# Performance work log

Measured on AMD Instinct MI355X. Metric: run time of the kernel, lower is better.

Reference implementation:

```python
import jax, jax.numpy as jnp
import numpy as np

N_NODES = 100000
N_EDGES = 1600000
IN_C, HID_C, OUT_C = 128, 128, 64


def setup_inputs() -> dict:
    key = jax.random.key(0)
    k1, k2, k3, k4 = jax.random.split(key, 4)
    x = jax.random.normal(k1, (N_NODES, IN_C), dtype=jnp.float32)
    edge_index = jax.random.randint(k2, (2, N_EDGES), 0, N_NODES, dtype=jnp.int32)
    # Glorot-ish init for linear weights, zero bias (PyG GCNConv default bias=0)
    W1 = jax.random.normal(k3, (IN_C, HID_C), dtype=jnp.float32) / np.sqrt(IN_C)
    b1 = jnp.zeros((HID_C,), dtype=jnp.float32)
    W2 = jax.random.normal(k4, (HID_C, OUT_C), dtype=jnp.float32) / np.sqrt(HID_C)
    b2 = jnp.zeros((OUT_C,), dtype=jnp.float32)
    return {"x": x, "edge_index": edge_index, "W1": W1, "b1": b1, "W2": W2, "b2": b2}


def gcn_conv(x, edge_index, W, b, n_nodes):
    """PyG GCNConv: out = D^{-1/2} (A + I) D^{-1/2} (x W) + b."""
    h = x @ W  # [N, C_out]
    loop = jnp.arange(n_nodes, dtype=edge_index.dtype)
    src = jnp.concatenate([edge_index[0], loop])  # messages flow src -> dst
    dst = jnp.concatenate([edge_index[1], loop])
    # degree at destination nodes (includes self-loops)
    deg = jax.ops.segment_sum(jnp.ones_like(src, dtype=h.dtype), dst,
                              num_segments=n_nodes)
    dis = jnp.where(deg > 0, jax.lax.rsqrt(jnp.maximum(deg, 1e-12)), 0.0)
    norm = dis[src] * dis[dst]  # [E+N]
    msg = h[src] * norm[:, None]  # gather + scale
    out = jax.ops.segment_sum(msg, dst, num_segments=n_nodes)  # scatter-add
    return out + b


def reference(x, edge_index, W1, b1, W2, b2):
    h = jax.nn.relu(gcn_conv(x, edge_index, W1, b1, N_NODES))
    return gcn_conv(h, edge_index, W2, b2, N_NODES)
```

## Files before the change

kernel.cpp:

```cpp
#include <hip/hip_runtime.h>

#define N_NODES 100000
#define N_EDGES 1600000
#define IN_C 128
#define HID_C 128
#define OUT_C 64

#define SH 8
#define NBKT 391
#define CAP 4608
#define EPB 4096
#define EPT 16

typedef __attribute__((ext_vector_type(8))) short bf16x8;
typedef __attribute__((ext_vector_type(4))) float f32x4;

static __device__ __forceinline__ unsigned f2bf(float f) {
  union { float f; unsigned u; } v; v.f = f;
  unsigned r = v.u + 0x7fffu + ((v.u >> 16) & 1u);
  return r >> 16;
}
static __device__ __forceinline__ float bf2f(unsigned hu) {
  union { unsigned u; float f; } v; v.u = hu << 16; return v.f;
}
static __device__ __forceinline__ float bflo(unsigned u) {
  union { unsigned u; float f; } v; v.u = u << 16; return v.f;
}
static __device__ __forceinline__ float bfhi(unsigned u) {
  union { unsigned u; float f; } v; v.u = u & 0xffff0000u; return v.f;
}


__global__ __launch_bounds__(256) void k_partA(const int* __restrict__ src,
                                               const int* __restrict__ dst,
                                               int* __restrict__ bcnt,
                                               unsigned* __restrict__ tmp, int e) {
  __shared__ unsigned stage[EPB];
  __shared__ unsigned short bid[EPB];
  __shared__ int hist[NBKT];
  __shared__ int lstart[NBKT];
  __shared__ int base[NBKT];
  __shared__ int ps[256];
  const int t = threadIdx.x;
  const int e0 = blockIdx.x * EPB;
  const int m = (e0 + EPB < e ? EPB : e - e0);

  for (int i = t; i < NBKT; i += 256) hist[i] = 0;
  __syncthreads();

  int rsrc[EPT], rdst[EPT];
#pragma unroll
  for (int i = 0; i < EPT; ++i) {
    int idx = e0 + i * 256 + t;
    if (idx < e) {
      rsrc[i] = src[idx];
      rdst[i] = dst[idx];
      atomicAdd(&hist[rdst[i] >> SH], 1);
    }
  }
  __syncthreads();

  int a0 = (2 * t < NBKT) ? hist[2 * t] : 0;
  int a1 = (2 * t + 1 < NBKT) ? hist[2 * t + 1] : 0;
  ps[t] = a0 + a1;
  __syncthreads();
  for (int off = 1; off < 256; off <<= 1) {
    int add = (t >= off) ? ps[t - off] : 0;
    __syncthreads();
    ps[t] += add;
    __syncthreads();
  }
  int ex = ps[t] - (a0 + a1);
  if (2 * t < NBKT) lstart[2 * t] = ex;
  if (2 * t + 1 < NBKT) lstart[2 * t + 1] = ex + a0;

  for (int i = t; i < NBKT; i += 256) {
    int h = hist[i];
    base[i] = h ? atomicAdd(&bcnt[i], h) : 0;
    hist[i] = 0;
  }
  __syncthreads();

#pragma unroll
  for (int i = 0; i < EPT; ++i) {
    int idx = e0 + i * 256 + t;
    if (idx < e) {
      int d = rdst[i];
      int b = d >> SH;
      int pos = lstart[b] + atomicAdd(&hist[b], 1);
      stage[pos] = (unsigned)rsrc[i] | ((unsigned)(d & 255) << 17);
      bid[pos] = (unsigned short)b;
    }
  }
  __syncthreads();

  for (int pos = t; pos < m; pos += 256) {
    int b = bid[pos];
    int slot = base[b] + (pos - lstart[b]);
    if (slot < CAP)
      tmp[(size_t)b * CAP + slot] = stage[pos];
  }
}

__global__ __launch_bounds__(256) void k_cnt_scan(const unsigned* __restrict__ tmp,
                                                  const int* __restrict__ bcnt,
                                                  int* __restrict__ rowptr,
                                                  int* __restrict__ bsums,
                                                  float* __restrict__ dis, int n) {
  __shared__ int h[256];
  __shared__ int s[256];
  const int b = blockIdx.x, t = threadIdx.x;
  h[t] = 0;
  __syncthreads();
  int m = bcnt[b];
  if (m > CAP) m = CAP;
  for (int j = t; j < m; j += 256)
    atomicAdd(&h[tmp[(size_t)b * CAP + j] >> 17], 1);
  __syncthreads();
  const int node = (b << SH) + t;
  int v = (node < n) ? h[t] : 0;
  if (node < n) dis[node] = rsqrtf((float)(v + 1));
  s[t] = v;
  __syncthreads();
  for (int off = 1; off < 256; off <<= 1) {
    int add = (t >= off) ? s[t - off] : 0;
    __syncthreads();
    s[t] += add;
    __syncthreads();
  }
  if (node < n) rowptr[node] = s[t] - v;
  if (t == 255) bsums[b] = s[255];
}

__global__ void k_scan_sums(int* __restrict__ bsums, int nb) {
  __shared__ int s[512];
  int t = threadIdx.x;
  int v = (t < nb) ? bsums[t] : 0;
  s[t] = v;
  __syncthreads();
  for (int off = 1; off < 512; off <<= 1) {
    int add = (t >= off) ? s[t - off] : 0;
    __syncthreads();
    s[t] += add;
    __syncthreads();
  }
  if (t < nb) bsums[t] = s[t] - v;
}

__global__ void k_add_off(int* __restrict__ rowptr, const int* __restrict__ bsums,
                          int n, int e) {
  int i = blockIdx.x * blockDim.x + threadIdx.x;
  if (i < n) rowptr[i] += bsums[i >> 8];
  else if (i == n) rowptr[n] = e;
}

__global__ __launch_bounds__(256) void k_partB(const unsigned* __restrict__ tmp,
                                               const int* __restrict__ bcnt,
                                               const int* __restrict__ rowptr,
                                               int* __restrict__ col, int n) {
  __shared__ int cur[256];
  const int b = blockIdx.x;
  const int t = threadIdx.x;
  const int node = (b << SH) + t;
  cur[t] = (node < n) ? rowptr[node] : 0;
  __syncthreads();
  int m = bcnt[b];
  if (m > CAP) m = CAP;
  for (int j = t; j < m; j += 256) {
    unsigned v = tmp[(size_t)b * CAP + j];
    int pos = atomicAdd(&cur[v >> 17], 1);
    col[pos] = (int)(v & 0x1FFFFu);
  }
}


__global__ void k_prepW(const float* __restrict__ W1, const float* __restrict__ W2,
                        unsigned short* __restrict__ W1h, unsigned short* __restrict__ W1l,
                        unsigned short* __restrict__ W2h, unsigned short* __restrict__ W2l) {
  int i = blockIdx.x * blockDim.x + threadIdx.x;
  if (i < IN_C * HID_C) {
    int k = i >> 7, c = i & 127;
    float w = W1[i];
    unsigned hi = f2bf(w);
    W1h[c * 128 + k] = (unsigned short)hi;
    W1l[c * 128 + k] = (unsigned short)f2bf(w - bf2f(hi));
  }
  int j = i - IN_C * HID_C;
  if (j >= 0 && j < HID_C * OUT_C) {
    int k = j >> 6, c = j & 63;
    float w = W2[j];
    unsigned hi = f2bf(w);
    W2h[c * 128 + k] = (unsigned short)hi;
    W2l[c * 128 + k] = (unsigned short)f2bf(w - bf2f(hi));
  }
}


__global__ __launch_bounds__(256) void k_mfma1(const float* __restrict__ X,
                                               const unsigned short* __restrict__ Wh,
                                               const unsigned short* __restrict__ Wl,
                                               const float* __restrict__ dis,
                                               unsigned short* __restrict__ Hs, int n) {
  __shared__ unsigned short xs[64 * 136];
  const int t = threadIdx.x;
  const int w = t >> 6, l = t & 63;
  const int lr = l & 15, lk = (l >> 4) * 8;
  const int row0 = blockIdx.x * 64;

  bf16x8 Bh[2][4], Bl[2][4];
#pragma unroll
  for (int c2 = 0; c2 < 2; ++c2)
#pragma unroll
    for (int kb = 0; kb < 4; ++kb) {
      int colw = w * 32 + c2 * 16 + lr;
      Bh[c2][kb] = *(const bf16x8*)&Wh[(size_t)colw * 128 + kb * 32 + lk];
      Bl[c2][kb] = *(const bf16x8*)&Wl[(size_t)colw * 128 + kb * 32 + lk];
    }

  for (int i = t; i < 64 * 32; i += 256) {
    int r = i >> 5, q = i & 31;
    float4 v = make_float4(0.f, 0.f, 0.f, 0.f);
    if (row0 + r < n) v = ((const float4*)(X + (size_t)(row0 + r) * IN_C))[q];
    unsigned p0 = f2bf(v.x) | (f2bf(v.y) << 16);
    unsigned p1 = f2bf(v.z) | (f2bf(v.w) << 16);
    *(uint2*)&xs[r * 136 + q * 4] = make_uint2(p0, p1);
  }
  __syncthreads();

#pragma unroll
  for (int rst = 0; rst < 4; ++rst) {
    bf16x8 a[4];
#pragma unroll
    for (int kb = 0; kb < 4; ++kb)
      a[kb] = *(const bf16x8*)&xs[(rst * 16 + lr) * 136 + kb * 32 + lk];
    f32x4 acc0 = (f32x4){0.f, 0.f, 0.f, 0.f};
    f32x4 acc1 = (f32x4){0.f, 0.f, 0.f, 0.f};
#pragma unroll
    for (int kb = 0; kb < 4; ++kb) {
      acc0 = __builtin_amdgcn_mfma_f32_16x16x32_bf16(a[kb], Bh[0][kb], acc0, 0, 0, 0);
      acc1 = __builtin_amdgcn_mfma_f32_16x16x32_bf16(a[kb], Bh[1][kb], acc1, 0, 0, 0);
      acc0 = __builtin_amdgcn_mfma_f32_16x16x32_bf16(a[kb], Bl[0][kb], acc0, 0, 0, 0);
      acc1 = __builtin_amdgcn_mfma_f32_16x16x32_bf16(a[kb], Bl[1][kb], acc1, 0, 0, 0);
    }
    const int rbase = row0 + rst * 16 + (l >> 4) * 4;
    float dv[4];
#pragma unroll
    for (int j = 0; j < 4; ++j) dv[j] = (rbase + j < n) ? dis[rbase + j] : 0.f;
#pragma unroll
    for (int c2 = 0; c2 < 2; ++c2) {
      int colw = w * 32 + c2 * 16 + lr;
      const f32x4& acc = c2 ? acc1 : acc0;
#pragma unroll
      for (int j = 0; j < 4; ++j) {
        int row = rbase + j;
        if (row < n) Hs[(size_t)row * HID_C + colw] = (unsigned short)f2bf(acc[j] * dv[j]);
      }
    }
  }
}


__global__ __launch_bounds__(256) void k_mfma2(const unsigned* __restrict__ G,
                                               const unsigned short* __restrict__ Wh,
                                               const unsigned short* __restrict__ Wl,
                                               const float* __restrict__ dis,
                                               unsigned short* __restrict__ Hs, int n) {
  __shared__ unsigned short xs[64 * 136];
  const int t = threadIdx.x;
  const int w = t >> 6, l = t & 63;
  const int lr = l & 15, lk = (l >> 4) * 8;
  const int row0 = blockIdx.x * 64;

  bf16x8 Bh[4], Bl[4];
#pragma unroll
  for (int kb = 0; kb < 4; ++kb) {
    int colw = w * 16 + lr;
    Bh[kb] = *(const bf16x8*)&Wh[(size_t)colw * 128 + kb * 32 + lk];
    Bl[kb] = *(const bf16x8*)&Wl[(size_t)colw * 128 + kb * 32 + lk];
  }

  for (int i = t; i < 64 * 32; i += 256) {
    int r = i >> 5, q = i & 31;
    uint2 v = make_uint2(0u, 0u);
    if (row0 + r < n) v = *(const uint2*)&G[(size_t)(row0 + r) * 64 + q * 2];
    *(uint2*)&xs[r * 136 + q * 4] = v;
  }
  __syncthreads();

#pragma unroll
  for (int rst = 0; rst < 4; ++rst) {
    bf16x8 a[4];
#pragma unroll
    for (int kb = 0; kb < 4; ++kb)
      a[kb] = *(const bf16x8*)&xs[(rst * 16 + lr) * 136 + kb * 32 + lk];
    f32x4 acc = (f32x4){0.f, 0.f, 0.f, 0.f};
#pragma unroll
    for (int kb = 0; kb < 4; ++kb) {
      acc = __builtin_amdgcn_mfma_f32_16x16x32_bf16(a[kb], Bh[kb], acc, 0, 0, 0);
      acc = __builtin_amdgcn_mfma_f32_16x16x32_bf16(a[kb], Bl[kb], acc, 0, 0, 0);
    }
    const int rbase = row0 + rst * 16 + (l >> 4) * 4;
    const int colw = w * 16 + lr;
#pragma unroll
    for (int j = 0; j < 4; ++j) {
      int row = rbase + j;
      if (row < n) Hs[(size_t)row * OUT_C + colw] =
          (unsigned short)f2bf(acc[j] * dis[row]);
    }
  }
}


__global__ __launch_bounds__(256) void k_agg128(const unsigned* __restrict__ Hs,
                                                const int* __restrict__ rowptr,
                                                const int* __restrict__ col,
                                                const float* __restrict__ dis,
                                                const float* __restrict__ bias,
                                                unsigned* __restrict__ G, int n) {
  const int node = (blockIdx.x * blockDim.x + threadIdx.x) >> 6;
  const int lane = threadIdx.x & 63;
  if (node >= n) return;
  const int g = lane >> 4, q = lane & 15;
  float a0 = 0.f, a1 = 0.f, a2 = 0.f, a3 = 0.f, a4 = 0.f, a5 = 0.f, a6 = 0.f, a7 = 0.f;
  const int beg = rowptr[node], end = rowptr[node + 1];
  int j = beg + g;
  for (; j + 8 <= end; j += 8) {
    int s0 = col[j], s1 = col[j + 4];
    uint4 v0 = *(const uint4*)&Hs[(size_t)s0 * 64 + q * 4];
    uint4 v1 = *(const uint4*)&Hs[(size_t)s1 * 64 + q * 4];
    a0 += bflo(v0.x) + bflo(v1.x); a1 += bfhi(v0.x) + bfhi(v1.x);
    a2 += bflo(v0.y) + bflo(v1.y); a3 += bfhi(v0.y) + bfhi(v1.y);
    a4 += bflo(v0.z) + bflo(v1.z); a5 += bfhi(v0.z) + bfhi(v1.z);
    a6 += bflo(v0.w) + bflo(v1.w); a7 += bfhi(v0.w) + bfhi(v1.w);
  }
  for (; j < end; j += 4) {
    int s = col[j];
    uint4 v = *(const uint4*)&Hs[(size_t)s * 64 + q * 4];
    a0 += bflo(v.x); a1 += bfhi(v.x);
    a2 += bflo(v.y); a3 += bfhi(v.y);
    a4 += bflo(v.z); a5 += bfhi(v.z);
    a6 += bflo(v.w); a7 += bfhi(v.w);
  }
  a0 += __shfl_xor(a0, 16, 64); a0 += __shfl_xor(a0, 32, 64);
  a1 += __shfl_xor(a1, 16, 64); a1 += __shfl_xor(a1, 32, 64);
  a2 += __shfl_xor(a2, 16, 64); a2 += __shfl_xor(a2, 32, 64);
  a3 += __shfl_xor(a3, 16, 64); a3 += __shfl_xor(a3, 32, 64);
  a4 += __shfl_xor(a4, 16, 64); a4 += __shfl_xor(a4, 32, 64);
  a5 += __shfl_xor(a5, 16, 64); a5 += __shfl_xor(a5, 32, 64);
  a6 += __shfl_xor(a6, 16, 64); a6 += __shfl_xor(a6, 32, 64);
  a7 += __shfl_xor(a7, 16, 64); a7 += __shfl_xor(a7, 32, 64);
  uint4 sv = *(const uint4*)&Hs[(size_t)node * 64 + q * 4];
  const float di = dis[node];
  const int c0 = q * 8;
  float2 b0 = *(const float2*)&bias[c0];
  float2 b1 = *(const float2*)&bias[c0 + 2];
  float2 b2 = *(const float2*)&bias[c0 + 4];
  float2 b3 = *(const float2*)&bias[c0 + 6];
  float r0 = fmaxf(fmaf(a0 + bflo(sv.x), di, b0.x), 0.f);
  float r1 = fmaxf(fmaf(a1 + bfhi(sv.x), di, b0.y), 0.f);
  float r2 = fmaxf(fmaf(a2 + bflo(sv.y), di, b1.x), 0.f);
  float r3 = fmaxf(fmaf(a3 + bfhi(sv.y), di, b1.y), 0.f);
  float r4 = fmaxf(fmaf(a4 + bflo(sv.z), di, b2.x), 0.f);
  float r5 = fmaxf(fmaf(a5 + bfhi(sv.z), di, b2.y), 0.f);
  float r6 = fmaxf(fmaf(a6 + bflo(sv.w), di, b3.x), 0.f);
  float r7 = fmaxf(fmaf(a7 + bfhi(sv.w), di, b3.y), 0.f);
  if (g == 0) {
    uint4 pk;
    pk.x = f2bf(r0) | (f2bf(r1) << 16);
    pk.y = f2bf(r2) | (f2bf(r3) << 16);
    pk.z = f2bf(r4) | (f2bf(r5) << 16);
    pk.w = f2bf(r6) | (f2bf(r7) << 16);
    *(uint4*)&G[(size_t)node * 64 + q * 4] = pk;
  }
}

__global__ __launch_bounds__(256) void k_agg64(const unsigned* __restrict__ Hs,
                                               const int* __restrict__ rowptr,
                                               const int* __restrict__ col,
                                               const float* __restrict__ dis,
                                               const float* __restrict__ bias,
                                               float* __restrict__ out, int n) {
  const int node = (blockIdx.x * blockDim.x + threadIdx.x) >> 6;
  const int lane = threadIdx.x & 63;
  if (node >= n) return;
  const int g = lane >> 4, q = lane & 15;
  float a0 = 0.f, a1 = 0.f, a2 = 0.f, a3 = 0.f;
  const int beg = rowptr[node], end = rowptr[node + 1];
  int j = beg + g;
  for (; j + 8 <= end; j += 8) {
    int s0 = col[j], s1 = col[j + 4];
    uint2 v0 = *(const uint2*)&Hs[(size_t)s0 * 32 + q * 2];
    uint2 v1 = *(const uint2*)&Hs[(size_t)s1 * 32 + q * 2];
    a0 += bflo(v0.x) + bflo(v1.x); a1 += bfhi(v0.x) + bfhi(v1.x);
    a2 += bflo(v0.y) + bflo(v1.y); a3 += bfhi(v0.y) + bfhi(v1.y);
  }
  for (; j < end; j += 4) {
    int s = col[j];
    uint2 v = *(const uint2*)&Hs[(size_t)s * 32 + q * 2];
    a0 += bflo(v.x); a1 += bfhi(v.x);
    a2 += bflo(v.y); a3 += bfhi(v.y);
  }
  a0 += __shfl_xor(a0, 16, 64); a0 += __shfl_xor(a0, 32, 64);
  a1 += __shfl_xor(a1, 16, 64); a1 += __shfl_xor(a1, 32, 64);
  a2 += __shfl_xor(a2, 16, 64); a2 += __shfl_xor(a2, 32, 64);
  a3 += __shfl_xor(a3, 16, 64); a3 += __shfl_xor(a3, 32, 64);
  uint2 sv = *(const uint2*)&Hs[(size_t)node * 32 + q * 2];
  const float di = dis[node];
  const int c0 = q * 4;
  float2 b0 = *(const float2*)&bias[c0];
  float2 b1 = *(const float2*)&bias[c0 + 2];
  if (g == 0) {
    float4 r;
    r.x = fmaf(a0 + bflo(sv.x), di, b0.x);
    r.y = fmaf(a1 + bfhi(sv.x), di, b0.y);
    r.z = fmaf(a2 + bflo(sv.y), di, b1.x);
    r.w = fmaf(a3 + bfhi(sv.y), di, b1.y);
    *(float4*)&out[(size_t)node * 64 + c0] = r;
  }
}


extern "C" void kernel_launch(void* const* d_in, const int* in_sizes, int n_in,
                              void* d_out, int out_size, void* d_ws, size_t ws_size,
                              hipStream_t stream) {
  const float* x  = (const float*)d_in[0];
  const int*   ei = (const int*)d_in[1];
  const float* W1 = (const float*)d_in[2];
  const float* b1 = (const float*)d_in[3];
  const float* W2 = (const float*)d_in[4];
  const float* b2 = (const float*)d_in[5];
  float* out = (float*)d_out;

  const int N = N_NODES, E = N_EDGES;
  const int* esrc = ei;
  const int* edst = ei + E;

  char* w = (char*)d_ws;
  auto alloc = [&](size_t bytes) -> char* {
    char* p = w;
    w += (bytes + 255) & ~(size_t)255;
    return p;
  };
  float* dis          = (float*)alloc((size_t)N * 4);
  int* rowptr         = (int*)alloc((size_t)(N + 1) * 4);
  int* bcnt           = (int*)alloc((size_t)NBKT * 4);
  int* bsums          = (int*)alloc(512 * 4);
  int* col            = (int*)alloc((size_t)E * 4);
  unsigned* tmp       = (unsigned*)alloc((size_t)NBKT * CAP * 4);
  unsigned short* h1s = (unsigned short*)alloc((size_t)N * HID_C * 2);
  unsigned* g1        = (unsigned*)alloc((size_t)N * (HID_C / 2) * 4);
  unsigned short* h2s = (unsigned short*)alloc((size_t)N * OUT_C * 2);
  unsigned short* W1h = (unsigned short*)alloc((size_t)IN_C * HID_C * 2);
  unsigned short* W1l = (unsigned short*)alloc((size_t)IN_C * HID_C * 2);
  unsigned short* W2h = (unsigned short*)alloc((size_t)HID_C * OUT_C * 2);
  unsigned short* W2l = (unsigned short*)alloc((size_t)HID_C * OUT_C * 2);

  hipMemsetAsync(bcnt, 0, (size_t)NBKT * 4, stream);
  k_partA<<<(E + EPB - 1) / EPB, 256, 0, stream>>>(esrc, edst, bcnt, tmp, E);
  k_cnt_scan<<<NBKT, 256, 0, stream>>>(tmp, bcnt, rowptr, bsums, dis, N);
  k_scan_sums<<<1, 512, 0, stream>>>(bsums, NBKT);
  k_add_off<<<(N + 1 + 255) / 256, 256, 0, stream>>>(rowptr, bsums, N, E);
  k_partB<<<NBKT, 256, 0, stream>>>(tmp, bcnt, rowptr, col, N);
  k_prepW<<<(IN_C * HID_C + HID_C * OUT_C + 255) / 256, 256, 0, stream>>>(
      W1, W2, W1h, W1l, W2h, W2l);

  k_mfma1<<<(N + 63) / 64, 256, 0, stream>>>(x, W1h, W1l, dis, h1s, N);
  k_agg128<<<(N * 64 + 255) / 256, 256, 0, stream>>>((const unsigned*)h1s, rowptr, col,
                                                     dis, b1, g1, N);
  k_mfma2<<<(N + 63) / 64, 256, 0, stream>>>(g1, W2h, W2l, dis, h2s, N);
  k_agg64<<<(N * 64 + 255) / 256, 256, 0, stream>>>((const unsigned*)h2s, rowptr, col,
                                                    dis, b2, out, N);
}
```

Measured before the change: 220.5 us.

## Unroll aggregation gathers, halve threads per node in agg64, widen partB

The 128-channel aggregation now unrolls to four independent row gathers per iteration, which puts more loads in flight. The 64-channel aggregation maps each node to 32 lanes instead of 64, so two edge groups per node replace four, with a 4-way unroll and a single shuffle reduction. The CSR fill kernel runs with 512 threads per block. More in-flight loads per lane could raise register pressure, and the agg64 remap halves the number of lanes working on each node's edge list.

Result: faster. 211.7 us (-4.0%).

```diff
diff --git a/kernel.cpp b/kernel.cpp
--- a/kernel.cpp
+++ b/kernel.cpp
@@ -154,19 +154,21 @@
   else if (i == n) rowptr[n] = e;
 }
 
-__global__ __launch_bounds__(256) void k_partB(const unsigned* __restrict__ tmp,
+__global__ __launch_bounds__(512) void k_partB(const unsigned* __restrict__ tmp,
                                                const int* __restrict__ bcnt,
                                                const int* __restrict__ rowptr,
                                                int* __restrict__ col, int n) {
   __shared__ int cur[256];
   const int b = blockIdx.x;
   const int t = threadIdx.x;
-  const int node = (b << SH) + t;
-  cur[t] = (node < n) ? rowptr[node] : 0;
+  if (t < 256) {
+    const int node = (b << SH) + t;
+    cur[t] = (node < n) ? rowptr[node] : 0;
+  }
   __syncthreads();
   int m = bcnt[b];
   if (m > CAP) m = CAP;
-  for (int j = t; j < m; j += 256) {
+  for (int j = t; j < m; j += 512) {
     unsigned v = tmp[(size_t)b * CAP + j];
     int pos = atomicAdd(&cur[v >> 17], 1);
     col[pos] = (int)(v & 0x1FFFFu);
@@ -324,14 +326,20 @@
   float a0 = 0.f, a1 = 0.f, a2 = 0.f, a3 = 0.f, a4 = 0.f, a5 = 0.f, a6 = 0.f, a7 = 0.f;
   const int beg = rowptr[node], end = rowptr[node + 1];
   int j = beg + g;
-  for (; j + 8 <= end; j += 8) {
-    int s0 = col[j], s1 = col[j + 4];
+  for (; j + 16 <= end; j += 16) {
+    int s0 = col[j], s1 = col[j + 4], s2 = col[j + 8], s3 = col[j + 12];
     uint4 v0 = *(const uint4*)&Hs[(size_t)s0 * 64 + q * 4];
     uint4 v1 = *(const uint4*)&Hs[(size_t)s1 * 64 + q * 4];
-    a0 += bflo(v0.x) + bflo(v1.x); a1 += bfhi(v0.x) + bfhi(v1.x);
-    a2 += bflo(v0.y) + bflo(v1.y); a3 += bfhi(v0.y) + bfhi(v1.y);
-    a4 += bflo(v0.z) + bflo(v1.z); a5 += bfhi(v0.z) + bfhi(v1.z);
-    a6 += bflo(v0.w) + bflo(v1.w); a7 += bfhi(v0.w) + bfhi(v1.w);
+    uint4 v2 = *(const uint4*)&Hs[(size_t)s2 * 64 + q * 4];
+    uint4 v3 = *(const uint4*)&Hs[(size_t)s3 * 64 + q * 4];
+    a0 += (bflo(v0.x) + bflo(v1.x)) + (bflo(v2.x) + bflo(v3.x));
+    a1 += (bfhi(v0.x) + bfhi(v1.x)) + (bfhi(v2.x) + bfhi(v3.x));
+    a2 += (bflo(v0.y) + bflo(v1.y)) + (bflo(v2.y) + bflo(v3.y));
+    a3 += (bfhi(v0.y) + bfhi(v1.y)) + (bfhi(v2.y) + bfhi(v3.y));
+    a4 += (bflo(v0.z) + bflo(v1.z)) + (bflo(v2.z) + bflo(v3.z));
+    a5 += (bfhi(v0.z) + bfhi(v1.z)) + (bfhi(v2.z) + bfhi(v3.z));
+    a6 += (bflo(v0.w) + bflo(v1.w)) + (bflo(v2.w) + bflo(v3.w));
+    a7 += (bfhi(v0.w) + bfhi(v1.w)) + (bfhi(v2.w) + bfhi(v3.w));
   }
   for (; j < end; j += 4) {
     int s = col[j];
@@ -356,15 +364,15 @@
   float2 b1 = *(const float2*)&bias[c0 + 2];
   float2 b2 = *(const float2*)&bias[c0 + 4];
   float2 b3 = *(const float2*)&bias[c0 + 6];
-  float r0 = fmaxf(fmaf(a0 + bflo(sv.x), di, b0.x), 0.f);
-  float r1 = fmaxf(fmaf(a1 + bfhi(sv.x), di, b0.y), 0.f);
-  float r2 = fmaxf(fmaf(a2 + bflo(sv.y), di, b1.x), 0.f);
-  float r3 = fmaxf(fmaf(a3 + bfhi(sv.y), di, b1.y), 0.f);
-  float r4 = fmaxf(fmaf(a4 + bflo(sv.z), di, b2.x), 0.f);
-  float r5 = fmaxf(fmaf(a5 + bfhi(sv.z), di, b2.y), 0.f);
-  float r6 = fmaxf(fmaf(a6 + bflo(sv.w), di, b3.x), 0.f);
-  float r7 = fmaxf(fmaf(a7 + bfhi(sv.w), di, b3.y), 0.f);
   if (g == 0) {
+    float r0 = fmaxf(fmaf(a0 + bflo(sv.x), di, b0.x), 0.f);
+    float r1 = fmaxf(fmaf(a1 + bfhi(sv.x), di, b0.y), 0.f);
+    float r2 = fmaxf(fmaf(a2 + bflo(sv.y), di, b1.x), 0.f);
+    float r3 = fmaxf(fmaf(a3 + bfhi(sv.y), di, b1.y), 0.f);
+    float r4 = fmaxf(fmaf(a4 + bflo(sv.z), di, b2.x), 0.f);
+    float r5 = fmaxf(fmaf(a5 + bfhi(sv.z), di, b2.y), 0.f);
+    float r6 = fmaxf(fmaf(a6 + bflo(sv.w), di, b3.x), 0.f);
+    float r7 = fmaxf(fmaf(a7 + bfhi(sv.w), di, b3.y), 0.f);
     uint4 pk;
     pk.x = f2bf(r0) | (f2bf(r1) << 16);
     pk.y = f2bf(r2) | (f2bf(r3) << 16);
@@ -380,30 +388,34 @@
                                                const float* __restrict__ dis,
                                                const float* __restrict__ bias,
                                                float* __restrict__ out, int n) {
-  const int node = (blockIdx.x * blockDim.x + threadIdx.x) >> 6;
-  const int lane = threadIdx.x & 63;
+  const int node = (blockIdx.x * blockDim.x + threadIdx.x) >> 5;
+  const int sub = threadIdx.x & 31;
   if (node >= n) return;
-  const int g = lane >> 4, q = lane & 15;
+  const int g = sub >> 4, q = sub & 15;
   float a0 = 0.f, a1 = 0.f, a2 = 0.f, a3 = 0.f;
   const int beg = rowptr[node], end = rowptr[node + 1];
   int j = beg + g;
   for (; j + 8 <= end; j += 8) {
-    int s0 = col[j], s1 = col[j + 4];
+    int s0 = col[j], s1 = col[j + 2], s2 = col[j + 4], s3 = col[j + 6];
     uint2 v0 = *(const uint2*)&Hs[(size_t)s0 * 32 + q * 2];
     uint2 v1 = *(const uint2*)&Hs[(size_t)s1 * 32 + q * 2];
-    a0 += bflo(v0.x) + bflo(v1.x); a1 += bfhi(v0.x) + bfhi(v1.x);
-    a2 += bflo(v0.y) + bflo(v1.y); a3 += bfhi(v0.y) + bfhi(v1.y);
-  }
-  for (; j < end; j += 4) {
+    uint2 v2 = *(const uint2*)&Hs[(size_t)s2 * 32 + q * 2];
+    uint2 v3 = *(const uint2*)&Hs[(size_t)s3 * 32 + q * 2];
+    a0 += (bflo(v0.x) + bflo(v1.x)) + (bflo(v2.x) + bflo(v3.x));
+    a1 += (bfhi(v0.x) + bfhi(v1.x)) + (bfhi(v2.x) + bfhi(v3.x));
+    a2 += (bflo(v0.y) + bflo(v1.y)) + (bflo(v2.y) + bflo(v3.y));
+    a3 += (bfhi(v0.y) + bfhi(v1.y)) + (bfhi(v2.y) + bfhi(v3.y));
+  }
+  for (; j < end; j += 2) {
     int s = col[j];
     uint2 v = *(const uint2*)&Hs[(size_t)s * 32 + q * 2];
     a0 += bflo(v.x); a1 += bfhi(v.x);
     a2 += bflo(v.y); a3 += bfhi(v.y);
   }
-  a0 += __shfl_xor(a0, 16, 64); a0 += __shfl_xor(a0, 32, 64);
-  a1 += __shfl_xor(a1, 16, 64); a1 += __shfl_xor(a1, 32, 64);
-  a2 += __shfl_xor(a2, 16, 64); a2 += __shfl_xor(a2, 32, 64);
-  a3 += __shfl_xor(a3, 16, 64); a3 += __shfl_xor(a3, 32, 64);
+  a0 += __shfl_xor(a0, 16, 64);
+  a1 += __shfl_xor(a1, 16, 64);
+  a2 += __shfl_xor(a2, 16, 64);
+  a3 += __shfl_xor(a3, 16, 64);
   uint2 sv = *(const uint2*)&Hs[(size_t)node * 32 + q * 2];
   const float di = dis[node];
   const int c0 = q * 4;
@@ -460,7 +472,7 @@
   k_cnt_scan<<<NBKT, 256, 0, stream>>>(tmp, bcnt, rowptr, bsums, dis, N);
   k_scan_sums<<<1, 512, 0, stream>>>(bsums, NBKT);
   k_add_off<<<(N + 1 + 255) / 256, 256, 0, stream>>>(rowptr, bsums, N, E);
-  k_partB<<<NBKT, 256, 0, stream>>>(tmp, bcnt, rowptr, col, N);
+  k_partB<<<NBKT, 512, 0, stream>>>(tmp, bcnt, rowptr, col, N);
   k_prepW<<<(IN_C * HID_C + HID_C * OUT_C + 255) / 256, 256, 0, stream>>>(
       W1, W2, W1h, W1l, W2h, W2l);
 
@@ -468,6 +480,6 @@
   k_agg128<<<(N * 64 + 255) / 256, 256, 0, stream>>>((const unsigned*)h1s, rowptr, col,
                                                      dis, b1, g1, N);
   k_mfma2<<<(N + 63) / 64, 256, 0, stream>>>(g1, W2h, W2l, dis, h2s, N);
-  k_agg64<<<(N * 64 + 255) / 256, 256, 0, stream>>>((const unsigned*)h2s, rowptr, col,
+  k_agg64<<<(N * 32 + 255) / 256, 256, 0, stream>>>((const unsigned*)h2s, rowptr, col,
                                                     dis, b2, out, N);
 }
```

## Split hidden features into column-group slabs and aggregate per group for cache locality

Applied to the files above, without the earlier changes.

The MFMA kernels now write their bf16 outputs as eight separate column-group slabs (16 or 8 channels each) instead of row-major rows. The aggregation kernels assign each block to one column group and 64 nodes, so every gather touches a small slab that fits better in L2/MALL. Column indices are read with nontemporal loads. The cost is that each edge list is now read eight times, with narrower per-lane loads, longer reduction shuffles and a serial loop over nodes per wave. k_partB also moves to 512 threads per block.

After: 652.1 us. +195.8%, slower.

```diff
diff --git a/kernel.cpp b/kernel.cpp
--- a/kernel.cpp
+++ b/kernel.cpp
@@ -154,19 +154,21 @@
   else if (i == n) rowptr[n] = e;
 }
 
-__global__ __launch_bounds__(256) void k_partB(const unsigned* __restrict__ tmp,
+__global__ __launch_bounds__(512) void k_partB(const unsigned* __restrict__ tmp,
                                                const int* __restrict__ bcnt,
                                                const int* __restrict__ rowptr,
                                                int* __restrict__ col, int n) {
   __shared__ int cur[256];
   const int b = blockIdx.x;
   const int t = threadIdx.x;
-  const int node = (b << SH) + t;
-  cur[t] = (node < n) ? rowptr[node] : 0;
+  if (t < 256) {
+    const int node = (b << SH) + t;
+    cur[t] = (node < n) ? rowptr[node] : 0;
+  }
   __syncthreads();
   int m = bcnt[b];
   if (m > CAP) m = CAP;
-  for (int j = t; j < m; j += 256) {
+  for (int j = t; j < m; j += 512) {
     unsigned v = tmp[(size_t)b * CAP + j];
     int pos = atomicAdd(&cur[v >> 17], 1);
     col[pos] = (int)(v & 0x1FFFFu);
@@ -200,7 +202,7 @@
                                                const unsigned short* __restrict__ Wh,
                                                const unsigned short* __restrict__ Wl,
                                                const float* __restrict__ dis,
-                                               unsigned short* __restrict__ Hs, int n) {
+                                               unsigned short* __restrict__ Hb, int n) {
   __shared__ unsigned short xs[64 * 136];
   const int t = threadIdx.x;
   const int w = t >> 6, l = t & 63;
@@ -248,12 +250,13 @@
     for (int j = 0; j < 4; ++j) dv[j] = (rbase + j < n) ? dis[rbase + j] : 0.f;
 #pragma unroll
     for (int c2 = 0; c2 < 2; ++c2) {
-      int colw = w * 32 + c2 * 16 + lr;
+      const int grp = w * 2 + c2;
       const f32x4& acc = c2 ? acc1 : acc0;
 #pragma unroll
       for (int j = 0; j < 4; ++j) {
         int row = rbase + j;
-        if (row < n) Hs[(size_t)row * HID_C + colw] = (unsigned short)f2bf(acc[j] * dv[j]);
+        if (row < n)
+          Hb[((size_t)grp * n + row) * 16 + lr] = (unsigned short)f2bf(acc[j] * dv[j]);
       }
     }
   }
@@ -264,7 +267,7 @@
                                                const unsigned short* __restrict__ Wh,
                                                const unsigned short* __restrict__ Wl,
                                                const float* __restrict__ dis,
-                                               unsigned short* __restrict__ Hs, int n) {
+                                               unsigned short* __restrict__ Hb, int n) {
   __shared__ unsigned short xs[64 * 136];
   const int t = threadIdx.x;
   const int w = t >> 6, l = t & 63;
@@ -301,121 +304,114 @@
     }
     const int rbase = row0 + rst * 16 + (l >> 4) * 4;
     const int colw = w * 16 + lr;
+    const int grp = colw >> 3;
+    const int within = colw & 7;
 #pragma unroll
     for (int j = 0; j < 4; ++j) {
       int row = rbase + j;
-      if (row < n) Hs[(size_t)row * OUT_C + colw] =
-          (unsigned short)f2bf(acc[j] * dis[row]);
-    }
-  }
-}
-
-
-__global__ __launch_bounds__(256) void k_agg128(const unsigned* __restrict__ Hs,
+      if (row < n)
+        Hb[((size_t)grp * n + row) * 8 + within] =
+            (unsigned short)f2bf(acc[j] * dis[row]);
+    }
+  }
+}
+
+
+__global__ __launch_bounds__(256) void k_agg128(const unsigned* __restrict__ Hb,
                                                 const int* __restrict__ rowptr,
                                                 const int* __restrict__ col,
                                                 const float* __restrict__ dis,
                                                 const float* __restrict__ bias,
                                                 unsigned* __restrict__ G, int n) {
-  const int node = (blockIdx.x * blockDim.x + threadIdx.x) >> 6;
-  const int lane = threadIdx.x & 63;
-  if (node >= n) return;
-  const int g = lane >> 4, q = lane & 15;
-  float a0 = 0.f, a1 = 0.f, a2 = 0.f, a3 = 0.f, a4 = 0.f, a5 = 0.f, a6 = 0.f, a7 = 0.f;
-  const int beg = rowptr[node], end = rowptr[node + 1];
-  int j = beg + g;
-  for (; j + 8 <= end; j += 8) {
-    int s0 = col[j], s1 = col[j + 4];
-    uint4 v0 = *(const uint4*)&Hs[(size_t)s0 * 64 + q * 4];
-    uint4 v1 = *(const uint4*)&Hs[(size_t)s1 * 64 + q * 4];
-    a0 += bflo(v0.x) + bflo(v1.x); a1 += bfhi(v0.x) + bfhi(v1.x);
-    a2 += bflo(v0.y) + bflo(v1.y); a3 += bfhi(v0.y) + bfhi(v1.y);
-    a4 += bflo(v0.z) + bflo(v1.z); a5 += bfhi(v0.z) + bfhi(v1.z);
-    a6 += bflo(v0.w) + bflo(v1.w); a7 += bfhi(v0.w) + bfhi(v1.w);
-  }
-  for (; j < end; j += 4) {
-    int s = col[j];
-    uint4 v = *(const uint4*)&Hs[(size_t)s * 64 + q * 4];
-    a0 += bflo(v.x); a1 += bfhi(v.x);
-    a2 += bflo(v.y); a3 += bfhi(v.y);
-    a4 += bflo(v.z); a5 += bfhi(v.z);
-    a6 += bflo(v.w); a7 += bfhi(v.w);
-  }
-  a0 += __shfl_xor(a0, 16, 64); a0 += __shfl_xor(a0, 32, 64);
-  a1 += __shfl_xor(a1, 16, 64); a1 += __shfl_xor(a1, 32, 64);
-  a2 += __shfl_xor(a2, 16, 64); a2 += __shfl_xor(a2, 32, 64);
-  a3 += __shfl_xor(a3, 16, 64); a3 += __shfl_xor(a3, 32, 64);
-  a4 += __shfl_xor(a4, 16, 64); a4 += __shfl_xor(a4, 32, 64);
-  a5 += __shfl_xor(a5, 16, 64); a5 += __shfl_xor(a5, 32, 64);
-  a6 += __shfl_xor(a6, 16, 64); a6 += __shfl_xor(a6, 32, 64);
-  a7 += __shfl_xor(a7, 16, 64); a7 += __shfl_xor(a7, 32, 64);
-  uint4 sv = *(const uint4*)&Hs[(size_t)node * 64 + q * 4];
-  const float di = dis[node];
-  const int c0 = q * 8;
-  float2 b0 = *(const float2*)&bias[c0];
-  float2 b1 = *(const float2*)&bias[c0 + 2];
-  float2 b2 = *(const float2*)&bias[c0 + 4];
-  float2 b3 = *(const float2*)&bias[c0 + 6];
-  float r0 = fmaxf(fmaf(a0 + bflo(sv.x), di, b0.x), 0.f);
-  float r1 = fmaxf(fmaf(a1 + bfhi(sv.x), di, b0.y), 0.f);
-  float r2 = fmaxf(fmaf(a2 + bflo(sv.y), di, b1.x), 0.f);
-  float r3 = fmaxf(fmaf(a3 + bfhi(sv.y), di, b1.y), 0.f);
-  float r4 = fmaxf(fmaf(a4 + bflo(sv.z), di, b2.x), 0.f);
-  float r5 = fmaxf(fmaf(a5 + bfhi(sv.z), di, b2.y), 0.f);
-  float r6 = fmaxf(fmaf(a6 + bflo(sv.w), di, b3.x), 0.f);
-  float r7 = fmaxf(fmaf(a7 + bfhi(sv.w), di, b3.y), 0.f);
-  if (g == 0) {
-    uint4 pk;
-    pk.x = f2bf(r0) | (f2bf(r1) << 16);
-    pk.y = f2bf(r2) | (f2bf(r3) << 16);
-    pk.z = f2bf(r4) | (f2bf(r5) << 16);
-    pk.w = f2bf(r6) | (f2bf(r7) << 16);
-    *(uint4*)&G[(size_t)node * 64 + q * 4] = pk;
-  }
-}
-
-__global__ __launch_bounds__(256) void k_agg64(const unsigned* __restrict__ Hs,
+  const int g = blockIdx.x & 7;
+  const int nb = blockIdx.x >> 3;
+  const int t = threadIdx.x;
+  const int w = t >> 6, l = t & 63;
+  const int slot = l >> 3, q = l & 7;
+  const unsigned* T = Hb + (size_t)g * n * 8;
+  const float2 bq = *(const float2*)&bias[g * 16 + q * 2];
+
+  for (int i = 0; i < 16; ++i) {
+    const int node = nb * 64 + w * 16 + i;
+    if (node >= n) return;
+    const int beg = rowptr[node], end = rowptr[node + 1];
+    float a0 = 0.f, a1 = 0.f;
+    int j0 = beg;
+    for (; j0 + 16 <= end; j0 += 16) {
+      int s0 = __builtin_nontemporal_load(&col[j0 + slot]);
+      int s1 = __builtin_nontemporal_load(&col[j0 + 8 + slot]);
+      unsigned u0 = T[(size_t)s0 * 8 + q];
+      unsigned u1 = T[(size_t)s1 * 8 + q];
+      a0 += bflo(u0) + bflo(u1);
+      a1 += bfhi(u0) + bfhi(u1);
+    }
+    for (; j0 < end; j0 += 8) {
+      int jj = j0 + slot;
+      if (jj < end) {
+        int s = __builtin_nontemporal_load(&col[jj]);
+        unsigned u = T[(size_t)s * 8 + q];
+        a0 += bflo(u);
+        a1 += bfhi(u);
+      }
+    }
+    a0 += __shfl_xor(a0, 8, 64); a0 += __shfl_xor(a0, 16, 64); a0 += __shfl_xor(a0, 32, 64);
+    a1 += __shfl_xor(a1, 8, 64); a1 += __shfl_xor(a1, 16, 64); a1 += __shfl_xor(a1, 32, 64);
+    const float di = dis[node];
+    if (slot == 0) {
+      unsigned su = T[(size_t)node * 8 + q];
+      float r0 = fmaxf(fmaf(a0 + bflo(su), di, bq.x), 0.f);
+      float r1 = fmaxf(fmaf(a1 + bfhi(su), di, bq.y), 0.f);
+      G[(size_t)node * 64 + g * 8 + q] = f2bf(r0) | (f2bf(r1) << 16);
+    }
+  }
+}
+
+__global__ __launch_bounds__(256) void k_agg64(const unsigned* __restrict__ Hb,
                                                const int* __restrict__ rowptr,
                                                const int* __restrict__ col,
                                                const float* __restrict__ dis,
                                                const float* __restrict__ bias,
                                                float* __restrict__ out, int n) {
-  const int node = (blockIdx.x * blockDim.x + threadIdx.x) >> 6;
-  const int lane = threadIdx.x & 63;
-  if (node >= n) return;
-  const int g = lane >> 4, q = lane & 15;
-  float a0 = 0.f, a1 = 0.f, a2 = 0.f, a3 = 0.f;
-  const int beg = rowptr[node], end = rowptr[node + 1];
-  int j = beg + g;
-  for (; j + 8 <= end; j += 8) {
-    int s0 = col[j], s1 = col[j + 4];
-    uint2 v0 = *(const uint2*)&Hs[(size_t)s0 * 32 + q * 2];
-    uint2 v1 = *(const uint2*)&Hs[(size_t)s1 * 32 + q * 2];
-    a0 += bflo(v0.x) + bflo(v1.x); a1 += bfhi(v0.x) + bfhi(v1.x);
-    a2 += bflo(v0.y) + bflo(v1.y); a3 += bfhi(v0.y) + bfhi(v1.y);
-  }
-  for (; j < end; j += 4) {
-    int s = col[j];
-    uint2 v = *(const uint2*)&Hs[(size_t)s * 32 + q * 2];
-    a0 += bflo(v.x); a1 += bfhi(v.x);
-    a2 += bflo(v.y); a3 += bfhi(v.y);
-  }
-  a0 += __shfl_xor(a0, 16, 64); a0 += __shfl_xor(a0, 32, 64);
-  a1 += __shfl_xor(a1, 16, 64); a1 += __shfl_xor(a1, 32, 64);
-  a2 += __shfl_xor(a2, 16, 64); a2 += __shfl_xor(a2, 32, 64);
-  a3 += __shfl_xor(a3, 16, 64); a3 += __shfl_xor(a3, 32, 64);
-  uint2 sv = *(const uint2*)&Hs[(size_t)node * 32 + q * 2];
-  const float di = dis[node];
-  const int c0 = q * 4;
-  float2 b0 = *(const float2*)&bias[c0];
-  float2 b1 = *(const float2*)&bias[c0 + 2];
-  if (g == 0) {
-    float4 r;
-    r.x = fmaf(a0 + bflo(sv.x), di, b0.x);
-    r.y = fmaf(a1 + bfhi(sv.x), di, b0.y);
-    r.z = fmaf(a2 + bflo(sv.y), di, b1.x);
-    r.w = fmaf(a3 + bfhi(sv.y), di, b1.y);
-    *(float4*)&out[(size_t)node * 64 + c0] = r;
+  const int g = blockIdx.x & 7;
+  const int nb = blockIdx.x >> 3;
+  const int t = threadIdx.x;
+  const int w = t >> 6, l = t & 63;
+  const int slot = l >> 2, q = l & 3;
+  const unsigned* T = Hb + (size_t)g * n * 4;
+  const float2 bq = *(const float2*)&bias[g * 8 + q * 2];
+
+  for (int i = 0; i < 16; ++i) {
+    const int node = nb * 64 + w * 16 + i;
+    if (node >= n) return;
+    const int beg = rowptr[node], end = rowptr[node + 1];
+    float a0 = 0.f, a1 = 0.f;
+    int j0 = beg;
+    for (; j0 + 16 <= end; j0 += 16) {
+      int s = __builtin_nontemporal_load(&col[j0 + slot]);
+      unsigned u = T[(size_t)s * 4 + q];
+      a0 += bflo(u);
+      a1 += bfhi(u);
+    }
+    if (j0 < end) {
+      int jj = j0 + slot;
+      if (jj < end) {
+        int s = __builtin_nontemporal_load(&col[jj]);
+        unsigned u = T[(size_t)s * 4 + q];
+        a0 += bflo(u);
+        a1 += bfhi(u);
+      }
+    }
+    a0 += __shfl_xor(a0, 4, 64); a0 += __shfl_xor(a0, 8, 64);
+    a0 += __shfl_xor(a0, 16, 64); a0 += __shfl_xor(a0, 32, 64);
+    a1 += __shfl_xor(a1, 4, 64); a1 += __shfl_xor(a1, 8, 64);
+    a1 += __shfl_xor(a1, 16, 64); a1 += __shfl_xor(a1, 32, 64);
+    const float di = dis[node];
+    if (slot == 0) {
+      unsigned su = T[(size_t)node * 4 + q];
+      float r0 = fmaf(a0 + bflo(su), di, bq.x);
+      float r1 = fmaf(a1 + bfhi(su), di, bq.y);
+      *(float2*)&out[(size_t)node * 64 + g * 8 + q * 2] = make_float2(r0, r1);
+    }
   }
 }
 
@@ -447,9 +443,9 @@
   int* bsums          = (int*)alloc(512 * 4);
   int* col            = (int*)alloc((size_t)E * 4);
   unsigned* tmp       = (unsigned*)alloc((size_t)NBKT * CAP * 4);
-  unsigned short* h1s = (unsigned short*)alloc((size_t)N * HID_C * 2);
+  unsigned short* h1b = (unsigned short*)alloc((size_t)8 * N * 16 * 2);
   unsigned* g1        = (unsigned*)alloc((size_t)N * (HID_C / 2) * 4);
-  unsigned short* h2s = (unsigned short*)alloc((size_t)N * OUT_C * 2);
+  unsigned short* h2b = (unsigned short*)alloc((size_t)8 * N * 8 * 2);
   unsigned short* W1h = (unsigned short*)alloc((size_t)IN_C * HID_C * 2);
   unsigned short* W1l = (unsigned short*)alloc((size_t)IN_C * HID_C * 2);
   unsigned short* W2h = (unsigned short*)alloc((size_t)HID_C * OUT_C * 2);
@@ -460,14 +456,14 @@
   k_cnt_scan<<<NBKT, 256, 0, stream>>>(tmp, bcnt, rowptr, bsums, dis, N);
   k_scan_sums<<<1, 512, 0, stream>>>(bsums, NBKT);
   k_add_off<<<(N + 1 + 255) / 256, 256, 0, stream>>>(rowptr, bsums, N, E);
-  k_partB<<<NBKT, 256, 0, stream>>>(tmp, bcnt, rowptr, col, N);
+  k_partB<<<NBKT, 512, 0, stream>>>(tmp, bcnt, rowptr, col, N);
   k_prepW<<<(IN_C * HID_C + HID_C * OUT_C + 255) / 256, 256, 0, stream>>>(
       W1, W2, W1h, W1l, W2h, W2l);
 
-  k_mfma1<<<(N + 63) / 64, 256, 0, stream>>>(x, W1h, W1l, dis, h1s, N);
-  k_agg128<<<(N * 64 + 255) / 256, 256, 0, stream>>>((const unsigned*)h1s, rowptr, col,
-                                                     dis, b1, g1, N);
-  k_mfma2<<<(N + 63) / 64, 256, 0, stream>>>(g1, W2h, W2l, dis, h2s, N);
-  k_agg64<<<(N * 64 + 255) / 256, 256, 0, stream>>>((const unsigned*)h2s, rowptr, col,
-                                                    dis, b2, out, N);
-}
+  const int aggGrid = ((N + 63) / 64) * 8;
+
+  k_mfma1<<<(N + 63) / 64, 256, 0, stream>>>(x, W1h, W1l, dis, h1b, N);
+  k_agg128<<<aggGrid, 256, 0, stream>>>((const unsigned*)h1b, rowptr, col, dis, b1, g1, N);
+  k_mfma2<<<(N + 63) / 64, 256, 0, stream>>>(g1, W2h, W2l, dis, h2b, N);
+  k_agg64<<<aggGrid, 256, 0, stream>>>((const unsigned*)h2b, rowptr, col, dis, b2, out, N);
+}
```
